# Optimization experiments

Measured on AMD Instinct MI355X. Metric: run time of the kernel, lower is better.

## Reference

```python
import jax, jax.numpy as jnp
import numpy as np


def setup_inputs() -> dict:
    key = jax.random.key(0)
    ks = jax.random.split(key, 5)
    B, S, D, H, DK, DV = 4, 2048, 1024, 16, 64, 64
    return {
        "x": jax.random.normal(ks[0], (B, S, D), dtype=jnp.float32),
        "W_q": jax.random.normal(ks[1], (H, D, DK), dtype=jnp.float32),
        "W_k": jax.random.normal(ks[2], (H, D, DK), dtype=jnp.float32),
        "W_v": jax.random.normal(ks[3], (H, D, DV), dtype=jnp.float32),
        "W_0": jax.random.normal(ks[4], (DV * H, D), dtype=jnp.float32),
    }


def reference(x, W_q, W_k, W_v, W_0):
    # x: [B, S, D]; W_q/W_k: [H, D, DK]; W_v: [H, D, DV]; W_0: [H*DV, D]
    B, S, D = x.shape
    H, _, DK = W_q.shape
    DV = W_v.shape[-1]
    Q = jnp.einsum("bsd,hdk->bhsk", x, W_q)
    K = jnp.einsum("bsd,hdk->bhsk", x, W_k)
    V = jnp.einsum("bsd,hdv->bhsv", x, W_v)
    scale = 1.0 / jnp.sqrt(jnp.asarray(DK, x.dtype))
    score = jnp.einsum("bhqk,bhsk->bhqs", Q, K) * scale  # [B,H,S,S]
    causal = jnp.tril(jnp.ones((S, S), dtype=bool))
    score = jnp.where(causal, score, -jnp.inf)
    attn = jax.nn.softmax(score, axis=-1)
    heads = jnp.einsum("bhqs,bhsv->bhqv", attn, V)  # [B,H,S,DV]
    # torch.cat along last dim in head order == transpose heads next to DV
    heads = heads.transpose(0, 2, 1, 3).reshape(B, S, H * DV)
    return heads @ W_0
```

## Files before the change

### kernel.cpp

```cpp
#include <hip/hip_runtime.h>

typedef __bf16 bf16;
typedef __bf16 bf16x4 __attribute__((ext_vector_type(4)));
typedef __bf16 bf16x8 __attribute__((ext_vector_type(8)));
typedef float  f32x2  __attribute__((ext_vector_type(2)));
typedef float  f32x4  __attribute__((ext_vector_type(4)));

#define NEG_INF (-__builtin_inff())
#define L2E 1.44269504088896f
#define DEFER_THR 5.545177444479562f


__global__ void k_cvt_wqkv(const float* __restrict__ wq, const float* __restrict__ wk,
                           const float* __restrict__ wv,
                           bf16* __restrict__ ohi, bf16* __restrict__ olo) {
    __shared__ float tile[64][65];
    const int d0 = blockIdx.x * 64, h = blockIdx.y, proj = blockIdx.z;
    const float* w = (proj == 0) ? wq : ((proj == 1) ? wk : wv);
    const int t = threadIdx.x;
    {
        int k = t & 63, dr = t >> 6;
        #pragma unroll
        for (int i = 0; i < 16; i++) {
            int dl = i * 4 + dr;
            tile[dl][k] = w[(size_t)(h * 1024 + d0 + dl) * 64 + k];
        }
    }
    __syncthreads();
    {
        int dl = t & 63, kr = t >> 6;
        #pragma unroll
        for (int i = 0; i < 16; i++) {
            int k = i * 4 + kr;
            float v = tile[dl][k];
            bf16 hi = (bf16)v;
            size_t o = (size_t)(proj * 1024 + h * 64 + k) * 1024 + d0 + dl;
            ohi[o] = hi;
            olo[o] = (bf16)(v - (float)hi);
        }
    }
}

__global__ void k_cvt_w0(const float* __restrict__ w0, bf16* __restrict__ out) {
    __shared__ float tile[64][65];
    const int n0 = blockIdx.x * 64, c0 = blockIdx.y * 64;
    const int t = threadIdx.x;
    {
        int n = t & 63, cr = t >> 6;
        #pragma unroll
        for (int i = 0; i < 16; i++) {
            int cl = i * 4 + cr;
            tile[cl][n] = w0[(size_t)(c0 + cl) * 1024 + n0 + n];
        }
    }
    __syncthreads();
    {
        int cl = t & 63, nr = t >> 6;
        #pragma unroll
        for (int i = 0; i < 16; i++) {
            int nl = i * 4 + nr;
            out[(size_t)(n0 + nl) * 1024 + c0 + cl] = (bf16)tile[cl][nl];
        }
    }
}

__global__ __launch_bounds__(256)
void k_gemm3(const float* __restrict__ A32,
             const bf16* __restrict__ Bhi, const bf16* __restrict__ Blo,
             bf16* __restrict__ Qhi, bf16* __restrict__ Qlo,
             bf16* __restrict__ Khi, bf16* __restrict__ Klo)
{
    __shared__ char Ash[128 * 128];
    __shared__ char Asl[128 * 128];
    __shared__ char Bsh[128 * 128];
    __shared__ char Bsl[128 * 128];
    const int t = threadIdx.x;
    const int m0 = blockIdx.x * 128;
    const int n0 = blockIdx.y * 128;
    const int wid = t >> 6, lane = t & 63, lr = lane & 15, lg = lane >> 4;
    const int wm = wid >> 1, wn = wid & 1;

    f32x4 acc[4][4] = {};

    for (int k0 = 0; k0 < 1024; k0 += 64) {
        #pragma unroll
        for (int i = 0; i < 4; i++) {
            int cid = t + i * 256;
            int r = cid >> 3, c8 = cid & 7;
            int sw = (c8 * 16) ^ ((r & 7) << 4);
            const float* ap = A32 + (size_t)(m0 + r) * 1024 + k0 + c8 * 8;
            float4 va = *reinterpret_cast<const float4*>(ap);
            float4 vb = *reinterpret_cast<const float4*>(ap + 4);
            float v[8] = {va.x, va.y, va.z, va.w, vb.x, vb.y, vb.z, vb.w};
            bf16x8 h8, l8;
            #pragma unroll
            for (int e = 0; e < 8; e++) {
                bf16 h = (bf16)v[e];
                h8[e] = h;
                l8[e] = (bf16)(v[e] - (float)h);
            }
            *reinterpret_cast<bf16x8*>(Ash + r * 128 + sw) = h8;
            *reinterpret_cast<bf16x8*>(Asl + r * 128 + sw) = l8;
            *reinterpret_cast<bf16x8*>(Bsh + r * 128 + sw) =
                *reinterpret_cast<const bf16x8*>(Bhi + (size_t)(n0 + r) * 1024 + k0 + c8 * 8);
            *reinterpret_cast<bf16x8*>(Bsl + r * 128 + sw) =
                *reinterpret_cast<const bf16x8*>(Blo + (size_t)(n0 + r) * 1024 + k0 + c8 * 8);
        }
        __syncthreads();
        #pragma unroll
        for (int kk = 0; kk < 2; kk++) {
            bf16x8 ah[4], al[4], bh[4], bl[4];
            #pragma unroll
            for (int mt = 0; mt < 4; mt++) {
                int row = wm * 64 + mt * 16 + lr;
                int off = row * 128 + (((kk * 4 + lg) * 16) ^ ((row & 7) << 4));
                ah[mt] = *reinterpret_cast<const bf16x8*>(Ash + off);
                al[mt] = *reinterpret_cast<const bf16x8*>(Asl + off);
            }
            #pragma unroll
            for (int nt = 0; nt < 4; nt++) {
                int row = wn * 64 + nt * 16 + lr;
                int off = row * 128 + (((kk * 4 + lg) * 16) ^ ((row & 7) << 4));
                bh[nt] = *reinterpret_cast<const bf16x8*>(Bsh + off);
                bl[nt] = *reinterpret_cast<const bf16x8*>(Bsl + off);
            }
            #pragma unroll
            for (int mt = 0; mt < 4; mt++)
                #pragma unroll
                for (int nt = 0; nt < 4; nt++) {
                    acc[mt][nt] = __builtin_amdgcn_mfma_f32_16x16x32_bf16(
                        ah[mt], bh[nt], acc[mt][nt], 0, 0, 0);
                    acc[mt][nt] = __builtin_amdgcn_mfma_f32_16x16x32_bf16(
                        ah[mt], bl[nt], acc[mt][nt], 0, 0, 0);
                    acc[mt][nt] = __builtin_amdgcn_mfma_f32_16x16x32_bf16(
                        al[mt], bh[nt], acc[mt][nt], 0, 0, 0);
                }
        }
        __syncthreads();
    }

    #pragma unroll
    for (int mt = 0; mt < 4; mt++)
        #pragma unroll
        for (int nt = 0; nt < 4; nt++)
            #pragma unroll
            for (int j = 0; j < 4; j++) {
                int m = m0 + wm * 64 + mt * 16 + lg * 4 + j;
                int n = n0 + wn * 64 + nt * 16 + lr;
                float v = acc[mt][nt][j];
                int b = m >> 11, s = m & 2047;
                if (n < 1024) {
                    int h = n >> 6, k = n & 63;
                    size_t idx = ((size_t)(b * 16 + h) * 2048 + s) * 64 + k;
                    float vs = v * 0.125f;
                    bf16 hi = (bf16)vs;
                    Qhi[idx] = hi;
                    Qlo[idx] = (bf16)(vs - (float)hi);
                } else {
                    int n2 = n - 1024, h = n2 >> 6, k = n2 & 63;
                    size_t idx = ((size_t)(b * 16 + h) * 2048 + s) * 64 + k;
                    bf16 hi = (bf16)v;
                    Khi[idx] = hi;
                    Klo[idx] = (bf16)(v - (float)hi);
                }
            }
}

__global__ __launch_bounds__(256)
void k_gemmV(const float* __restrict__ A32, const bf16* __restrict__ Bhi,
             bf16* __restrict__ Vtb)
{
    __shared__ char As[128 * 128];
    __shared__ char Bs[128 * 128];
    const int t = threadIdx.x;
    const int m0 = blockIdx.x * 128;
    const int nb = blockIdx.y * 128;
    const int wid = t >> 6, lane = t & 63, lr = lane & 15, lg = lane >> 4;
    const int wm = wid >> 1, wn = wid & 1;

    f32x4 acc[4][4] = {};

    for (int k0 = 0; k0 < 1024; k0 += 64) {
        #pragma unroll
        for (int i = 0; i < 4; i++) {
            int cid = t + i * 256;
            int r = cid >> 3, c8 = cid & 7;
            int sw = (c8 * 16) ^ ((r & 7) << 4);
            const float* ap = A32 + (size_t)(m0 + r) * 1024 + k0 + c8 * 8;
            float4 va = *reinterpret_cast<const float4*>(ap);
            float4 vb = *reinterpret_cast<const float4*>(ap + 4);
            float v[8] = {va.x, va.y, va.z, va.w, vb.x, vb.y, vb.z, vb.w};
            bf16x8 h8;
            #pragma unroll
            for (int e = 0; e < 8; e++) h8[e] = (bf16)v[e];
            *reinterpret_cast<bf16x8*>(As + r * 128 + sw) = h8;
            *reinterpret_cast<bf16x8*>(Bs + r * 128 + sw) =
                *reinterpret_cast<const bf16x8*>(Bhi + (size_t)(2048 + nb + r) * 1024 + k0 + c8 * 8);
        }
        __syncthreads();
        #pragma unroll
        for (int kk = 0; kk < 2; kk++) {
            bf16x8 af[4], bfr[4];
            #pragma unroll
            for (int mt = 0; mt < 4; mt++) {
                int row = wm * 64 + mt * 16 + lr;
                af[mt] = *reinterpret_cast<const bf16x8*>(
                    As + row * 128 + (((kk * 4 + lg) * 16) ^ ((row & 7) << 4)));
            }
            #pragma unroll
            for (int nt = 0; nt < 4; nt++) {
                int row = wn * 64 + nt * 16 + lr;
                bfr[nt] = *reinterpret_cast<const bf16x8*>(
                    Bs + row * 128 + (((kk * 4 + lg) * 16) ^ ((row & 7) << 4)));
            }
            #pragma unroll
            for (int mt = 0; mt < 4; mt++)
                #pragma unroll
                for (int nt = 0; nt < 4; nt++)
                    acc[mt][nt] = __builtin_amdgcn_mfma_f32_16x16x32_bf16(
                        af[mt], bfr[nt], acc[mt][nt], 0, 0, 0);
        }
        __syncthreads();
    }

    #pragma unroll
    for (int mt = 0; mt < 4; mt++)
        #pragma unroll
        for (int nt = 0; nt < 4; nt++)
            #pragma unroll
            for (int j = 0; j < 4; j++) {
                int m = m0 + wm * 64 + mt * 16 + lg * 4 + j;
                int nl = nb + wn * 64 + nt * 16 + lr;
                int b = m >> 11, s = m & 2047;
                int h = nl >> 6, dv = nl & 63;
                Vtb[((size_t)(b * 16 + h) * 64 + dv) * 2048 + s] = (bf16)acc[mt][nt][j];
            }
}

__global__ __launch_bounds__(256)
void k_gemm1(const bf16* __restrict__ A, const bf16* __restrict__ Bt,
             float* __restrict__ Out)
{
    __shared__ char As[128 * 128];
    __shared__ char Bs[128 * 128];
    const int t = threadIdx.x;
    const int m0 = blockIdx.x * 128;
    const int n0 = blockIdx.y * 128;
    const int wid = t >> 6, lane = t & 63, lr = lane & 15, lg = lane >> 4;
    const int wm = wid >> 1, wn = wid & 1;

    f32x4 acc[4][4] = {};

    for (int k0 = 0; k0 < 1024; k0 += 64) {
        #pragma unroll
        for (int i = 0; i < 4; i++) {
            int cid = t + i * 256;
            int r = cid >> 3, c8 = cid & 7;
            int sw = (c8 * 16) ^ ((r & 7) << 4);
            *reinterpret_cast<bf16x8*>(As + r * 128 + sw) =
                *reinterpret_cast<const bf16x8*>(A + (size_t)(m0 + r) * 1024 + k0 + c8 * 8);
            *reinterpret_cast<bf16x8*>(Bs + r * 128 + sw) =
                *reinterpret_cast<const bf16x8*>(Bt + (size_t)(n0 + r) * 1024 + k0 + c8 * 8);
        }
        __syncthreads();
        #pragma unroll
        for (int kk = 0; kk < 2; kk++) {
            bf16x8 af[4], bfr[4];
            #pragma unroll
            for (int mt = 0; mt < 4; mt++) {
                int row = wm * 64 + mt * 16 + lr;
                af[mt] = *reinterpret_cast<const bf16x8*>(
                    As + row * 128 + (((kk * 4 + lg) * 16) ^ ((row & 7) << 4)));
            }
            #pragma unroll
            for (int nt = 0; nt < 4; nt++) {
                int row = wn * 64 + nt * 16 + lr;
                bfr[nt] = *reinterpret_cast<const bf16x8*>(
                    Bs + row * 128 + (((kk * 4 + lg) * 16) ^ ((row & 7) << 4)));
            }
            #pragma unroll
            for (int mt = 0; mt < 4; mt++)
                #pragma unroll
                for (int nt = 0; nt < 4; nt++)
                    acc[mt][nt] = __builtin_amdgcn_mfma_f32_16x16x32_bf16(
                        af[mt], bfr[nt], acc[mt][nt], 0, 0, 0);
        }
        __syncthreads();
    }

    #pragma unroll
    for (int mt = 0; mt < 4; mt++)
        #pragma unroll
        for (int nt = 0; nt < 4; nt++)
            #pragma unroll
            for (int j = 0; j < 4; j++) {
                int m = m0 + wm * 64 + mt * 16 + lg * 4 + j;
                int n = n0 + wn * 64 + nt * 16 + lr;
                Out[(size_t)m * 1024 + n] = acc[mt][nt][j];
            }
}

__global__ __launch_bounds__(512, 4)
void k_attn(const bf16* __restrict__ Qhi, const bf16* __restrict__ Qlo,
            const bf16* __restrict__ Khi, const bf16* __restrict__ Klo,
            const bf16* __restrict__ Vtb, bf16* __restrict__ hd)
{
    __shared__ char LDS[49152];
    const int bid = blockIdx.x;
    const int x7 = bid & 7, k7 = bid >> 3;
    const int hh = k7 >> 4, q4 = k7 & 15;
    const int qB = 15 - q4;
    const int bh = x7 * 8 + hh;
    const int t = threadIdx.x, wid = t >> 6, lane = t & 63, lr = lane & 15, lg = lane >> 4;
    const bf16* Qhp = Qhi + (size_t)bh * 131072;
    const bf16* Qlp = Qlo + (size_t)bh * 131072;
    const int q0 = qB * 128 + wid * 16;
    const int qdiv = q0 >> 6;
    const int kbmax = 2 * qB + 1;
    const int qg = q0 + lr;

    bf16x8 qh[2], ql[2];
    #pragma unroll
    for (int kk = 0; kk < 2; kk++) {
        size_t off = (size_t)(q0 + lr) * 64 + kk * 32 + lg * 8;
        qh[kk] = *reinterpret_cast<const bf16x8*>(Qhp + off);
        ql[kk] = *reinterpret_cast<const bf16x8*>(Qlp + off);
    }

    const int swc = (lr & 7) << 4;
    const int b0 = lr * 128 + ((lg * 16) ^ swc);
    const int b1 = lr * 128 + ((64 + lg * 16) ^ swc);

    const int r = t >> 3, c8 = t & 7;
    const int wb = r * 128 + ((c8 * 16) ^ ((r & 7) << 4));
    const bf16* gk = Khi + (size_t)bh * 131072 + r * 64 + c8 * 8;
    const bf16* gl = Klo + (size_t)bh * 131072 + r * 64 + c8 * 8;
    const bf16* gv = Vtb + (size_t)bh * 131072 + r * 2048 + c8 * 8;

    {
        bf16x8 a = *reinterpret_cast<const bf16x8*>(gk);
        bf16x8 b = *reinterpret_cast<const bf16x8*>(gl);
        bf16x8 c = *reinterpret_cast<const bf16x8*>(gv);
        *reinterpret_cast<bf16x8*>(LDS + wb) = a;
        *reinterpret_cast<bf16x8*>(LDS + wb + 8192) = b;
        *reinterpret_cast<bf16x8*>(LDS + wb + 16384) = c;
    }
    __syncthreads();

    f32x4 accO[4] = {};
    float mrow = NEG_INF;
    float negmL2 = NEG_INF;
    f32x2 lsum2 = {0.0f, 0.0f};

    for (int kb = 0; kb <= kbmax; kb++) {
        const int ro = (kb & 1) ? 24576 : 0;
        const int wo = 24576 - ro;
        bf16x8 pkh, pkl, pv;
        if (kb < kbmax) {
            gk += 4096; gl += 4096; gv += 64;
            pkh = *reinterpret_cast<const bf16x8*>(gk);
            pkl = *reinterpret_cast<const bf16x8*>(gl);
            pv  = *reinterpret_cast<const bf16x8*>(gv);
        }

        if (kb <= qdiv) {
            const int bA = b0 + ro, bB = b1 + ro;
            f32x4 sc[4] = {};
            __builtin_amdgcn_s_setprio(1);
            #pragma unroll
            for (int kk = 0; kk < 2; kk++) {
                const int bb = kk ? bB : bA;
                bf16x8 bh8[4], bl8[4];
                #pragma unroll
                for (int nt = 0; nt < 4; nt++) {
                    bh8[nt] = *reinterpret_cast<const bf16x8*>(LDS + bb + nt * 2048);
                    bl8[nt] = *reinterpret_cast<const bf16x8*>(LDS + bb + nt * 2048 + 8192);
                }
                #pragma unroll
                for (int nt = 0; nt < 4; nt++) {
                    sc[nt] = __builtin_amdgcn_mfma_f32_16x16x32_bf16(bh8[nt], qh[kk], sc[nt], 0, 0, 0);
                    sc[nt] = __builtin_amdgcn_mfma_f32_16x16x32_bf16(bl8[nt], qh[kk], sc[nt], 0, 0, 0);
                    sc[nt] = __builtin_amdgcn_mfma_f32_16x16x32_bf16(bh8[nt], ql[kk], sc[nt], 0, 0, 0);
                }
            }
            __builtin_amdgcn_s_setprio(0);

            if (kb == qdiv) {
                #pragma unroll
                for (int nt = 0; nt < 4; nt++)
                    #pragma unroll
                    for (int j = 0; j < 4; j++) {
                        int kg = kb * 64 + nt * 16 + 4 * lg + j;
                        if (kg > qg) sc[nt][j] = NEG_INF;
                    }
            }

            float mA = fmaxf(fmaxf(sc[0][0], sc[0][1]), sc[0][2]);
            float mB = fmaxf(fmaxf(sc[0][3], sc[1][0]), sc[1][1]);
            float mC = fmaxf(fmaxf(sc[1][2], sc[1][3]), sc[2][0]);
            float mD = fmaxf(fmaxf(sc[2][1], sc[2][2]), sc[2][3]);
            float mE = fmaxf(fmaxf(sc[3][0], sc[3][1]), sc[3][2]);
            float lm = fmaxf(fmaxf(fmaxf(mA, mB), fmaxf(mC, mD)),
                             fmaxf(mE, sc[3][3]));
            if (__any(lm > mrow + DEFER_THR)) {
                float pm = lm;
                pm = fmaxf(pm, __shfl_xor(pm, 16));
                pm = fmaxf(pm, __shfl_xor(pm, 32));
                float mnew = fmaxf(mrow, pm);
                float alpha = __builtin_amdgcn_exp2f((mrow - mnew) * L2E);
                mrow = mnew;
                negmL2 = -mnew * L2E;
                lsum2 *= alpha;
                #pragma unroll
                for (int nt = 0; nt < 4; nt++)
                    #pragma unroll
                    for (int j = 0; j < 4; j++)
                        accO[nt][j] *= alpha;
            }

            f32x2 pr[8];
            #pragma unroll
            for (int nt = 0; nt < 4; nt++) {
                pr[2 * nt]     = __builtin_shufflevector(sc[nt], sc[nt], 0, 1);
                pr[2 * nt + 1] = __builtin_shufflevector(sc[nt], sc[nt], 2, 3);
            }
            const f32x2 vL2E = {L2E, L2E};
            const f32x2 vneg = {negmL2, negmL2};
            f32x2 ts2 = {0.0f, 0.0f};
            #pragma unroll
            for (int i = 0; i < 8; i++) {
                f32x2 a = __builtin_elementwise_fma(pr[i], vL2E, vneg);
                f32x2 e;
                e.x = __builtin_amdgcn_exp2f(a.x);
                e.y = __builtin_amdgcn_exp2f(a.y);
                pr[i] = e;
                ts2 += e;
            }
            lsum2 += ts2;

            unsigned int w[4][2];
            #pragma unroll
            for (int nt = 0; nt < 4; nt++)
                #pragma unroll
                for (int p = 0; p < 2; p++) {
                    unsigned int d;
                    asm("v_cvt_pk_bf16_f32 %0, %1, %2"
                        : "=v"(d) : "v"(pr[2 * nt + p].x), "v"(pr[2 * nt + p].y));
                    w[nt][p] = d;
                }
            bf16x8 bp[2];
            #pragma unroll
            for (int kk = 0; kk < 2; kk++) {
                unsigned int a0 = w[2 * kk][0], bq0 = w[2 * kk + 1][0];
                unsigned int a1 = w[2 * kk][1], bq1 = w[2 * kk + 1][1];
                asm("v_permlane32_swap_b32 %0, %1" : "+v"(a0), "+v"(bq0));
                asm("v_permlane16_swap_b32 %0, %1" : "+v"(a0), "+v"(bq0));
                asm("v_permlane32_swap_b32 %0, %1" : "+v"(a1), "+v"(bq1));
                asm("v_permlane16_swap_b32 %0, %1" : "+v"(a1), "+v"(bq1));
                union { unsigned int u[4]; bf16x8 v; } cvt;
                cvt.u[0] = a0; cvt.u[1] = a1; cvt.u[2] = bq0; cvt.u[3] = bq1;
                bp[kk] = cvt.v;
            }

            __builtin_amdgcn_s_setprio(1);
            #pragma unroll
            for (int kk = 0; kk < 2; kk++) {
                const int bb = kk ? bB : bA;
                #pragma unroll
                for (int nt = 0; nt < 4; nt++) {
                    bf16x8 bv = *reinterpret_cast<const bf16x8*>(LDS + bb + nt * 2048 + 16384);
                    accO[nt] = __builtin_amdgcn_mfma_f32_16x16x32_bf16(bv, bp[kk], accO[nt], 0, 0, 0);
                }
            }
            __builtin_amdgcn_s_setprio(0);
        }

        if (kb < kbmax) {
            *reinterpret_cast<bf16x8*>(LDS + wb + wo) = pkh;
            *reinterpret_cast<bf16x8*>(LDS + wb + wo + 8192) = pkl;
            *reinterpret_cast<bf16x8*>(LDS + wb + wo + 16384) = pv;
        }
        __syncthreads();
    }

    float ps = lsum2.x + lsum2.y;
    ps += __shfl_xor(ps, 16);
    ps += __shfl_xor(ps, 32);
    float inv = 1.0f / ps;
    size_t rowbase = (size_t)((bh >> 4) * 2048 + qg) * 1024 + (bh & 15) * 64;
    #pragma unroll
    for (int nt = 0; nt < 4; nt++) {
        bf16x4 o;
        #pragma unroll
        for (int j = 0; j < 4; j++) o[j] = (bf16)(accO[nt][j] * inv);
        *reinterpret_cast<bf16x4*>(hd + rowbase + nt * 16 + 4 * lg) = o;
    }
}


extern "C" void kernel_launch(void* const* d_in, const int* in_sizes, int n_in,
                              void* d_out, int out_size, void* d_ws, size_t ws_size,
                              hipStream_t stream) {
    const float* x  = (const float*)d_in[0];
    const float* Wq = (const float*)d_in[1];
    const float* Wk = (const float*)d_in[2];
    const float* Wv = (const float*)d_in[3];
    const float* W0 = (const float*)d_in[4];
    float* out = (float*)d_out;

    char* ws = (char*)d_ws;
    bf16* w0t = (bf16*)(ws + 0);
    bf16* Qhi = (bf16*)(ws + 2097152);
    bf16* Qlo = (bf16*)(ws + 18874368);
    bf16* Khi = (bf16*)(ws + 35651584);
    bf16* Klo = (bf16*)(ws + 52428800);
    bf16* Vtb = (bf16*)(ws + 69206016);
    bf16* whi = (bf16*)(ws + 85983232);
    bf16* wlo = (bf16*)(ws + 92274688);
    bf16* hd  = (bf16*)(ws + 85983232);
    if (ws_size < 102760448u) return;

    k_cvt_wqkv<<<dim3(16, 16, 3), 256, 0, stream>>>(Wq, Wk, Wv, whi, wlo);
    k_cvt_w0  <<<dim3(16, 16), 256, 0, stream>>>(W0, w0t);
    k_gemm3   <<<dim3(64, 16), 256, 0, stream>>>(x, whi, wlo, Qhi, Qlo, Khi, Klo);
    k_gemmV   <<<dim3(64, 8), 256, 0, stream>>>(x, whi, Vtb);
    k_attn    <<<1024, 512, 0, stream>>>(Qhi, Qlo, Khi, Klo, Vtb, hd);
    k_gemm1   <<<dim3(64, 8), 256, 0, stream>>>(hd, w0t, out);
}
```

Baseline: 284.5 us.

## Pre-split x into bf16 hi/lo and load GEMM tiles via global_load_lds

Adds a kernel that splits x into bf16 hi and lo planes once, stored temporarily in the output buffer. The QK and V projection GEMMs then read these bf16 planes instead of converting fp32 to bf16 inside every tile load, which the QK GEMM had repeated for each of its 16 column blocks. All GEMMs now stage tiles with direct global-to-LDS loads using a pre-swizzled lane address, bypassing registers. The V and output GEMMs are merged into one templated kernel. The cost is an extra pass over x and extra workspace traffic, and the output buffer is borrowed as scratch before the final GEMM overwrites it.

```diff
diff --git a/kernel.cpp b/kernel.cpp
--- a/kernel.cpp
+++ b/kernel.cpp
@@ -9,6 +9,28 @@
 #define NEG_INF (-__builtin_inff())
 #define L2E 1.44269504088896f
 #define DEFER_THR 5.545177444479562f
+
+__device__ __forceinline__ void gl16(const void* g, void* l) {
+    __builtin_amdgcn_global_load_lds(
+        (const __attribute__((address_space(1))) void*)g,
+        (__attribute__((address_space(3))) void*)l, 16, 0, 0);
+}
+
+__global__ void k_split_x(const float* __restrict__ x,
+                          bf16* __restrict__ xh, bf16* __restrict__ xl) {
+    int i = (blockIdx.x * 256 + threadIdx.x) * 4;
+    float4 v = *reinterpret_cast<const float4*>(x + i);
+    float a[4] = {v.x, v.y, v.z, v.w};
+    bf16x4 h, l;
+    #pragma unroll
+    for (int e = 0; e < 4; e++) {
+        bf16 hh = (bf16)a[e];
+        h[e] = hh;
+        l[e] = (bf16)(a[e] - (float)hh);
+    }
+    *reinterpret_cast<bf16x4*>(xh + i) = h;
+    *reinterpret_cast<bf16x4*>(xl + i) = l;
+}
 
 
 __global__ void k_cvt_wqkv(const float* __restrict__ wq, const float* __restrict__ wk,
@@ -65,46 +87,36 @@
 }
 
 __global__ __launch_bounds__(256)
-void k_gemm3(const float* __restrict__ A32,
-             const bf16* __restrict__ Bhi, const bf16* __restrict__ Blo,
+void k_gemm3(const bf16* __restrict__ Ah, const bf16* __restrict__ Al,
+             const bf16* __restrict__ Bh, const bf16* __restrict__ Bl,
              bf16* __restrict__ Qhi, bf16* __restrict__ Qlo,
              bf16* __restrict__ Khi, bf16* __restrict__ Klo)
 {
-    __shared__ char Ash[128 * 128];
-    __shared__ char Asl[128 * 128];
-    __shared__ char Bsh[128 * 128];
-    __shared__ char Bsl[128 * 128];
+    __shared__ char LDS[65536];
     const int t = threadIdx.x;
     const int m0 = blockIdx.x * 128;
     const int n0 = blockIdx.y * 128;
     const int wid = t >> 6, lane = t & 63, lr = lane & 15, lg = lane >> 4;
     const int wm = wid >> 1, wn = wid & 1;
 
+    const int eoff = (lane >> 3) * 1024 + (((lane & 7) ^ (lane >> 3)) * 8);
+    const bf16* pAh = Ah + (size_t)m0 * 1024 + eoff;
+    const bf16* pAl = Al + (size_t)m0 * 1024 + eoff;
+    const bf16* pBh = Bh + (size_t)n0 * 1024 + eoff;
+    const bf16* pBl = Bl + (size_t)n0 * 1024 + eoff;
+
     f32x4 acc[4][4] = {};
 
     for (int k0 = 0; k0 < 1024; k0 += 64) {
         #pragma unroll
         for (int i = 0; i < 4; i++) {
-            int cid = t + i * 256;
-            int r = cid >> 3, c8 = cid & 7;
-            int sw = (c8 * 16) ^ ((r & 7) << 4);
-            const float* ap = A32 + (size_t)(m0 + r) * 1024 + k0 + c8 * 8;
-            float4 va = *reinterpret_cast<const float4*>(ap);
-            float4 vb = *reinterpret_cast<const float4*>(ap + 4);
-            float v[8] = {va.x, va.y, va.z, va.w, vb.x, vb.y, vb.z, vb.w};
-            bf16x8 h8, l8;
-            #pragma unroll
-            for (int e = 0; e < 8; e++) {
-                bf16 h = (bf16)v[e];
-                h8[e] = h;
-                l8[e] = (bf16)(v[e] - (float)h);
-            }
-            *reinterpret_cast<bf16x8*>(Ash + r * 128 + sw) = h8;
-            *reinterpret_cast<bf16x8*>(Asl + r * 128 + sw) = l8;
-            *reinterpret_cast<bf16x8*>(Bsh + r * 128 + sw) =
-                *reinterpret_cast<const bf16x8*>(Bhi + (size_t)(n0 + r) * 1024 + k0 + c8 * 8);
-            *reinterpret_cast<bf16x8*>(Bsl + r * 128 + sw) =
-                *reinterpret_cast<const bf16x8*>(Blo + (size_t)(n0 + r) * 1024 + k0 + c8 * 8);
+            const int r0 = (wid * 4 + i) * 8;
+            const size_t gofs = (size_t)r0 * 1024 + k0;
+            char* ld = LDS + r0 * 128;
+            gl16(pAh + gofs, ld);
+            gl16(pAl + gofs, ld + 16384);
+            gl16(pBh + gofs, ld + 32768);
+            gl16(pBl + gofs, ld + 49152);
         }
         __syncthreads();
         #pragma unroll
@@ -114,15 +126,15 @@
             for (int mt = 0; mt < 4; mt++) {
                 int row = wm * 64 + mt * 16 + lr;
                 int off = row * 128 + (((kk * 4 + lg) * 16) ^ ((row & 7) << 4));
-                ah[mt] = *reinterpret_cast<const bf16x8*>(Ash + off);
-                al[mt] = *reinterpret_cast<const bf16x8*>(Asl + off);
+                ah[mt] = *reinterpret_cast<const bf16x8*>(LDS + off);
+                al[mt] = *reinterpret_cast<const bf16x8*>(LDS + 16384 + off);
             }
             #pragma unroll
             for (int nt = 0; nt < 4; nt++) {
                 int row = wn * 64 + nt * 16 + lr;
                 int off = row * 128 + (((kk * 4 + lg) * 16) ^ ((row & 7) << 4));
-                bh[nt] = *reinterpret_cast<const bf16x8*>(Bsh + off);
-                bl[nt] = *reinterpret_cast<const bf16x8*>(Bsl + off);
+                bh[nt] = *reinterpret_cast<const bf16x8*>(LDS + 32768 + off);
+                bl[nt] = *reinterpret_cast<const bf16x8*>(LDS + 49152 + off);
             }
             #pragma unroll
             for (int mt = 0; mt < 4; mt++)
@@ -166,101 +178,32 @@
             }
 }
 
+template<int MODE>
 __global__ __launch_bounds__(256)
-void k_gemmV(const float* __restrict__ A32, const bf16* __restrict__ Bhi,
-             bf16* __restrict__ Vtb)
+void k_gemm2(const bf16* __restrict__ A, const bf16* __restrict__ Bt,
+             bf16* __restrict__ Vtb, float* __restrict__ Out)
 {
-    __shared__ char As[128 * 128];
-    __shared__ char Bs[128 * 128];
-    const int t = threadIdx.x;
-    const int m0 = blockIdx.x * 128;
-    const int nb = blockIdx.y * 128;
-    const int wid = t >> 6, lane = t & 63, lr = lane & 15, lg = lane >> 4;
-    const int wm = wid >> 1, wn = wid & 1;
-
-    f32x4 acc[4][4] = {};
-
-    for (int k0 = 0; k0 < 1024; k0 += 64) {
-        #pragma unroll
-        for (int i = 0; i < 4; i++) {
-            int cid = t + i * 256;
-            int r = cid >> 3, c8 = cid & 7;
-            int sw = (c8 * 16) ^ ((r & 7) << 4);
-            const float* ap = A32 + (size_t)(m0 + r) * 1024 + k0 + c8 * 8;
-            float4 va = *reinterpret_cast<const float4*>(ap);
-            float4 vb = *reinterpret_cast<const float4*>(ap + 4);
-            float v[8] = {va.x, va.y, va.z, va.w, vb.x, vb.y, vb.z, vb.w};
-            bf16x8 h8;
-            #pragma unroll
-            for (int e = 0; e < 8; e++) h8[e] = (bf16)v[e];
-            *reinterpret_cast<bf16x8*>(As + r * 128 + sw) = h8;
-            *reinterpret_cast<bf16x8*>(Bs + r * 128 + sw) =
-                *reinterpret_cast<const bf16x8*>(Bhi + (size_t)(2048 + nb + r) * 1024 + k0 + c8 * 8);
-        }
-        __syncthreads();
-        #pragma unroll
-        for (int kk = 0; kk < 2; kk++) {
-            bf16x8 af[4], bfr[4];
-            #pragma unroll
-            for (int mt = 0; mt < 4; mt++) {
-                int row = wm * 64 + mt * 16 + lr;
-                af[mt] = *reinterpret_cast<const bf16x8*>(
-                    As + row * 128 + (((kk * 4 + lg) * 16) ^ ((row & 7) << 4)));
-            }
-            #pragma unroll
-            for (int nt = 0; nt < 4; nt++) {
-                int row = wn * 64 + nt * 16 + lr;
-                bfr[nt] = *reinterpret_cast<const bf16x8*>(
-                    Bs + row * 128 + (((kk * 4 + lg) * 16) ^ ((row & 7) << 4)));
-            }
-            #pragma unroll
-            for (int mt = 0; mt < 4; mt++)
-                #pragma unroll
-                for (int nt = 0; nt < 4; nt++)
-                    acc[mt][nt] = __builtin_amdgcn_mfma_f32_16x16x32_bf16(
-                        af[mt], bfr[nt], acc[mt][nt], 0, 0, 0);
-        }
-        __syncthreads();
-    }
-
-    #pragma unroll
-    for (int mt = 0; mt < 4; mt++)
-        #pragma unroll
-        for (int nt = 0; nt < 4; nt++)
-            #pragma unroll
-            for (int j = 0; j < 4; j++) {
-                int m = m0 + wm * 64 + mt * 16 + lg * 4 + j;
-                int nl = nb + wn * 64 + nt * 16 + lr;
-                int b = m >> 11, s = m & 2047;
-                int h = nl >> 6, dv = nl & 63;
-                Vtb[((size_t)(b * 16 + h) * 64 + dv) * 2048 + s] = (bf16)acc[mt][nt][j];
-            }
-}
-
-__global__ __launch_bounds__(256)
-void k_gemm1(const bf16* __restrict__ A, const bf16* __restrict__ Bt,
-             float* __restrict__ Out)
-{
-    __shared__ char As[128 * 128];
-    __shared__ char Bs[128 * 128];
+    __shared__ char LDS[32768];
     const int t = threadIdx.x;
     const int m0 = blockIdx.x * 128;
     const int n0 = blockIdx.y * 128;
     const int wid = t >> 6, lane = t & 63, lr = lane & 15, lg = lane >> 4;
     const int wm = wid >> 1, wn = wid & 1;
 
+    const int eoff = (lane >> 3) * 1024 + (((lane & 7) ^ (lane >> 3)) * 8);
+    const bf16* pA = A + (size_t)m0 * 1024 + eoff;
+    const bf16* pB = Bt + (size_t)n0 * 1024 + eoff;
+
     f32x4 acc[4][4] = {};
 
     for (int k0 = 0; k0 < 1024; k0 += 64) {
         #pragma unroll
         for (int i = 0; i < 4; i++) {
-            int cid = t + i * 256;
-            int r = cid >> 3, c8 = cid & 7;
-            int sw = (c8 * 16) ^ ((r & 7) << 4);
-            *reinterpret_cast<bf16x8*>(As + r * 128 + sw) =
-                *reinterpret_cast<const bf16x8*>(A + (size_t)(m0 + r) * 1024 + k0 + c8 * 8);
-            *reinterpret_cast<bf16x8*>(Bs + r * 128 + sw) =
-                *reinterpret_cast<const bf16x8*>(Bt + (size_t)(n0 + r) * 1024 + k0 + c8 * 8);
+            const int r0 = (wid * 4 + i) * 8;
+            const size_t gofs = (size_t)r0 * 1024 + k0;
+            char* ld = LDS + r0 * 128;
+            gl16(pA + gofs, ld);
+            gl16(pB + gofs, ld + 16384);
         }
         __syncthreads();
         #pragma unroll
@@ -270,13 +213,13 @@
             for (int mt = 0; mt < 4; mt++) {
                 int row = wm * 64 + mt * 16 + lr;
                 af[mt] = *reinterpret_cast<const bf16x8*>(
-                    As + row * 128 + (((kk * 4 + lg) * 16) ^ ((row & 7) << 4)));
+                    LDS + row * 128 + (((kk * 4 + lg) * 16) ^ ((row & 7) << 4)));
             }
             #pragma unroll
             for (int nt = 0; nt < 4; nt++) {
                 int row = wn * 64 + nt * 16 + lr;
                 bfr[nt] = *reinterpret_cast<const bf16x8*>(
-                    Bs + row * 128 + (((kk * 4 + lg) * 16) ^ ((row & 7) << 4)));
+                    LDS + 16384 + row * 128 + (((kk * 4 + lg) * 16) ^ ((row & 7) << 4)));
             }
             #pragma unroll
             for (int mt = 0; mt < 4; mt++)
@@ -295,8 +238,14 @@
             #pragma unroll
             for (int j = 0; j < 4; j++) {
                 int m = m0 + wm * 64 + mt * 16 + lg * 4 + j;
-                int n = n0 + wn * 64 + nt * 16 + lr;
-                Out[(size_t)m * 1024 + n] = acc[mt][nt][j];
+                int nl = n0 + wn * 64 + nt * 16 + lr;
+                if (MODE == 0) {
+                    int b = m >> 11, s = m & 2047;
+                    int h = nl >> 6, dv = nl & 63;
+                    Vtb[((size_t)(b * 16 + h) * 64 + dv) * 2048 + s] = (bf16)acc[mt][nt][j];
+                } else {
+                    Out[(size_t)m * 1024 + nl] = acc[mt][nt][j];
+                }
             }
 }
 
@@ -520,10 +469,14 @@
     bf16* hd  = (bf16*)(ws + 85983232);
     if (ws_size < 102760448u) return;
 
+    bf16* xh = (bf16*)d_out;
+    bf16* xl = xh + 8388608;
+
+    k_split_x <<<8192, 256, 0, stream>>>(x, xh, xl);
     k_cvt_wqkv<<<dim3(16, 16, 3), 256, 0, stream>>>(Wq, Wk, Wv, whi, wlo);
     k_cvt_w0  <<<dim3(16, 16), 256, 0, stream>>>(W0, w0t);
-    k_gemm3   <<<dim3(64, 16), 256, 0, stream>>>(x, whi, wlo, Qhi, Qlo, Khi, Klo);
-    k_gemmV   <<<dim3(64, 8), 256, 0, stream>>>(x, whi, Vtb);
+    k_gemm3   <<<dim3(64, 16), 256, 0, stream>>>(xh, xl, whi, wlo, Qhi, Qlo, Khi, Klo);
+    k_gemm2<0><<<dim3(64, 8), 256, 0, stream>>>(xh, whi + 2048 * 1024, Vtb, nullptr);
     k_attn    <<<1024, 512, 0, stream>>>(Qhi, Qlo, Khi, Klo, Vtb, hd);
-    k_gemm1   <<<dim3(64, 8), 256, 0, stream>>>(hd, w0t, out);
-}
+    k_gemm2<1><<<dim3(64, 8), 256, 0, stream>>>(hd, w0t, nullptr, out);
+}
```

Result: faster. 266.8 us (-6.2%).
